# Kernel optimization log

Hardware: AMD Instinct MI355X
Metric: run time of the kernel (lower is better)

The kernel has to match this reference:

```python
import jax, jax.numpy as jnp
import numpy as np

M, K = 16384, 1024
E, N = 8, 5632  # N = 2 * intermediate (gate+up packed); intermediate = 2816
TOPK = 2


def setup_inputs() -> dict:
    key = jax.random.key(0)
    ks = jax.random.split(key, 5)
    return {
        "hidden_states": jax.random.normal(ks[0], (M, K), jnp.float32) * 0.05,
        "w1": jax.random.normal(ks[1], (E, N, K), jnp.float32) * 0.02,
        "w2": jax.random.normal(ks[2], (E, K, N // 2), jnp.float32) * 0.02,
        "topk_weights": jax.random.uniform(ks[3], (M, TOPK), jnp.float32),
        "topk_ids": jax.random.randint(ks[4], (M, TOPK), 0, E, jnp.int32),
    }


def reference(hidden_states, w1, w2, topk_weights, topk_ids):
    # hidden_states: [M, K]; w1: [E, N, K]; w2: [E, K, N//2]
    # topk_weights / topk_ids: [M, TOPK]
    m, k = hidden_states.shape
    e_num, n, _ = w1.shape
    topk = topk_ids.shape[1]
    half = n // 2
    out = jnp.zeros((m, topk, k), dtype=hidden_states.dtype)
    # Loop over the small fixed set of experts; each iteration is a dense GEMM
    # masked by the routing assignment (faithful to the grouped-GEMM math).
    for e in range(e_num):
        h1 = jnp.einsum('mk,nk->mn', hidden_states, w1[e])          # [M, N]
        gate, up = h1[:, :half], h1[:, half:]
        h2 = jax.nn.silu(gate) * up                                  # silu_and_mul
        o = jnp.einsum('mh,kh->mk', h2, w2[e])                       # [M, K]
        mask = (topk_ids == e).astype(o.dtype)                       # [M, TOPK]
        out = out + mask[:, :, None] * o[:, None, :]
    # multiply routed weights and sum over top-k slots
    return jnp.einsum('mtk,mt->mk', out, topk_weights)
```

## Files before the change

### kernel.cpp

```cpp
#include <hip/hip_runtime.h>
#include <hip/hip_bf16.h>

#define M_TOK 16384
#define K_DIM 1024
#define E_NUM 8
#define N_DIM 5632
#define HALF_N 2816
#define TOPK 2
#define NPAIR (M_TOK * TOPK)
#define BM 128
#define BK 64
#define BH1 128
#define BN 128
#define NDESC (NPAIR / BM + E_NUM)
#define NHB1 (HALF_N / BH1)
#define NNB2 (K_DIM / BN)

typedef short s16x4 __attribute__((ext_vector_type(4)));
typedef short s16x8 __attribute__((ext_vector_type(8)));
typedef float f32x4 __attribute__((ext_vector_type(4)));

__device__ __forceinline__ short f2bf(float f) {
  union { __hip_bfloat16 h; short s; } c;
  c.h = __float2bfloat16(f);
  return c.s;
}

__device__ __forceinline__ float bf2f(unsigned short s) {
  union { float f; unsigned u; } c;
  c.u = ((unsigned)s) << 16;
  return c.f;
}

__device__ __forceinline__ void gload_lds16(const void* g, void* l) {
  __builtin_amdgcn_global_load_lds(
      (const __attribute__((address_space(1))) unsigned int*)g,
      (__attribute__((address_space(3))) unsigned int*)l, 16, 0, 0);
}

__device__ __forceinline__ int xcd_work(int bid, int nwg) {
  const int xcd = bid & 7, loc = bid >> 3;
  const int q = nwg >> 3, r = nwg & 7;
  return (xcd < r ? xcd * (q + 1) : r * (q + 1) + (xcd - r) * q) + loc;
}

__global__ void cvt_f32_bf16_k(const float4* __restrict__ src,
                               s16x4* __restrict__ dst, int n4) {
  int i = blockIdx.x * blockDim.x + threadIdx.x;
  int stride = gridDim.x * blockDim.x;
  for (; i < n4; i += stride) {
    float4 f = src[i];
    s16x4 o = { f2bf(f.x), f2bf(f.y), f2bf(f.z), f2bf(f.w) };
    dst[i] = o;
  }
}

__global__ void moe_count(const int* __restrict__ ids, int* __restrict__ cnt) {
  const int p = blockIdx.x * 256 + threadIdx.x;
  const int e = ids[p];
  const int lane = threadIdx.x & 63;
  __shared__ int h[E_NUM];
  if (threadIdx.x < E_NUM) h[threadIdx.x] = 0;
  __syncthreads();
#pragma unroll
  for (int ex = 0; ex < E_NUM; ++ex) {
    unsigned long long m = __ballot(e == ex);
    if (lane == 0 && m) atomicAdd(&h[ex], __popcll(m));
  }
  __syncthreads();
  if (threadIdx.x < E_NUM) atomicAdd(&cnt[threadIdx.x], h[threadIdx.x]);
}

__global__ void moe_build(const int* __restrict__ cnt, int* __restrict__ offs,
                          int4* __restrict__ desc) {
  if (blockIdx.x == 0 && threadIdx.x == 0) {
    int o = 0, d = 0;
    for (int e = 0; e < E_NUM; ++e) {
      offs[e] = o;
      int end = o + cnt[e];
      for (int s = o; s < end; s += BM) desc[d++] = make_int4(e, s, end, 0);
      o = end;
    }
    offs[E_NUM] = o;
    while (d < NDESC) desc[d++] = make_int4(-1, 0, 0, 0);
  }
}

__global__ void moe_scatter(const int* __restrict__ ids, const float* __restrict__ tw,
                            const int* __restrict__ offs, int* __restrict__ fill,
                            int* __restrict__ tok, float* __restrict__ wgt,
                            int* __restrict__ inv) {
  const int p = blockIdx.x * 256 + threadIdx.x;
  const int e = ids[p];
  const int lane = threadIdx.x & 63;
  const int w = threadIdx.x >> 6;
  __shared__ int wcnt[4][E_NUM];
  __shared__ int wpre[4][E_NUM];
  __shared__ int base[E_NUM];
  const unsigned long long lt = (1ull << lane) - 1ull;
  int myrank = 0;
#pragma unroll
  for (int ex = 0; ex < E_NUM; ++ex) {
    unsigned long long m = __ballot(e == ex);
    if (e == ex) myrank = (int)__popcll(m & lt);
    if (lane == 0) wcnt[w][ex] = (int)__popcll(m);
  }
  __syncthreads();
  if (threadIdx.x < E_NUM) {
    const int ex = threadIdx.x;
    int s = 0;
#pragma unroll
    for (int ww = 0; ww < 4; ++ww) { wpre[ww][ex] = s; s += wcnt[ww][ex]; }
    base[ex] = atomicAdd(&fill[ex], s);
  }
  __syncthreads();
  const int pos = offs[e] + base[e] + wpre[w][e] + myrank;
  tok[pos] = p >> 1;
  wgt[pos] = tw[p];
  inv[p] = pos;
}

__global__ void moe_gather(const float* __restrict__ hs, const int* __restrict__ tok,
                           unsigned short* __restrict__ hsb) {
  const int pos = blockIdx.x;
  const int m = tok[pos];
  const int t = threadIdx.x;
  const float4* s = (const float4*)(hs + (size_t)m * K_DIM) + t * 2;
  const float4 a = s[0], b = s[1];
  s16x8 o = { f2bf(a.x), f2bf(a.y), f2bf(a.z), f2bf(a.w),
              f2bf(b.x), f2bf(b.y), f2bf(b.z), f2bf(b.w) };
  *(s16x8*)(hsb + (size_t)pos * K_DIM + t * 8) = o;
}

__launch_bounds__(512)
__global__ void moe_gemm1(const unsigned short* __restrict__ hsb,
                          const unsigned short* __restrict__ w1b,
                          const int4* __restrict__ desc,
                          unsigned short* __restrict__ h2) {
  const int work = xcd_work(blockIdx.x, NHB1 * NDESC);
  const int di = work / NHB1;
  const int hb = work - di * NHB1;
  const int4 d = desc[di];
  const int e = d.x;
  if (e < 0) return;
  const int pos0 = d.y, eend = d.z;
  const int h0 = hb * BH1;

  __shared__ __align__(16) unsigned short As[BM * BK];
  __shared__ __align__(16) unsigned short Gs[BH1 * BK];
  __shared__ __align__(16) unsigned short Us[BH1 * BK];

  const int tid = threadIdx.x;
  const int lane = tid & 63;
  const int wid = tid >> 6;
  const int wr = wid >> 2;
  const int wc = wid & 3;

  const unsigned short* Ab = hsb + (size_t)pos0 * K_DIM;
  const unsigned short* Gb = w1b + ((size_t)e * N_DIM + h0) * K_DIM;
  const unsigned short* Ub = Gb + (size_t)HALF_N * K_DIM;

  f32x4 accg[4][2], accu[4][2];
  const f32x4 z = {0.f, 0.f, 0.f, 0.f};
#pragma unroll
  for (int i = 0; i < 4; ++i)
#pragma unroll
    for (int j = 0; j < 2; ++j) { accg[i][j] = z; accu[i][j] = z; }

  const int lrow = lane >> 3;
  const int scol = ((lane & 7) ^ lrow) << 3;
  const int fr = lane & 15;
  const int fq = lane >> 4;
  const int sw = fr & 7;

  for (int kt = 0; kt < K_DIM / BK; ++kt) {
    const int k0 = kt * BK;
#pragma unroll
    for (int c = 0; c < 2; ++c) {
      const int seg = c * 8 + wid;
      const int row = seg * 8 + lrow;
      gload_lds16(Ab + (size_t)row * K_DIM + k0 + scol, &As[seg * 512]);
      gload_lds16(Gb + (size_t)row * K_DIM + k0 + scol, &Gs[seg * 512]);
      gload_lds16(Ub + (size_t)row * K_DIM + k0 + scol, &Us[seg * 512]);
    }
    __syncthreads();
#pragma unroll
    for (int s = 0; s < 2; ++s) {
      const int coff = (((s * 4 + fq) ^ sw) << 3);
      s16x8 af[4];
#pragma unroll
      for (int i = 0; i < 4; ++i)
        af[i] = *(const s16x8*)&As[(64 * wr + 16 * i + fr) * BK + coff];
      s16x8 gf[2], uf[2];
#pragma unroll
      for (int j = 0; j < 2; ++j) {
        const int hr = (32 * wc + 16 * j + fr) * BK + coff;
        gf[j] = *(const s16x8*)&Gs[hr];
        uf[j] = *(const s16x8*)&Us[hr];
      }
#pragma unroll
      for (int i = 0; i < 4; ++i)
#pragma unroll
        for (int j = 0; j < 2; ++j) {
          accg[i][j] = __builtin_amdgcn_mfma_f32_16x16x32_bf16(af[i], gf[j], accg[i][j], 0, 0, 0);
          accu[i][j] = __builtin_amdgcn_mfma_f32_16x16x32_bf16(af[i], uf[j], accu[i][j], 0, 0, 0);
        }
    }
    __syncthreads();
  }

  const int vlim = eend - pos0;
#pragma unroll
  for (int i = 0; i < 4; ++i) {
#pragma unroll
    for (int rr = 0; rr < 4; ++rr) {
      const int row = 64 * wr + 16 * i + fq * 4 + rr;
      if (row < vlim) {
        unsigned short* dst = h2 + (size_t)(pos0 + row) * HALF_N + h0 + 32 * wc;
#pragma unroll
        for (int j = 0; j < 2; ++j) {
          const float g = accg[i][j][rr];
          const float u = accu[i][j][rr];
          const float sg = g / (1.0f + __expf(-g));
          dst[16 * j + fr] = (unsigned short)f2bf(sg * u);
        }
      }
    }
  }
}

__launch_bounds__(256)
__global__ void moe_gemm2(const unsigned short* __restrict__ h2,
                          const unsigned short* __restrict__ w2b,
                          const int4* __restrict__ desc,
                          const float* __restrict__ wgt,
                          unsigned short* __restrict__ opair) {
  const int work = xcd_work(blockIdx.x, NNB2 * NDESC);
  const int di = work >> 3;
  const int nb = work & 7;
  const int4 d = desc[di];
  const int e = d.x;
  if (e < 0) return;
  const int pos0 = d.y, eend = d.z;
  const int n0 = nb * BN;

  __shared__ __align__(16) unsigned short As[BM * BK];
  __shared__ __align__(16) unsigned short Bs[BN * BK];

  const int tid = threadIdx.x;
  const int lane = tid & 63;
  const int wid = tid >> 6;
  const int wr = wid >> 1, wc = wid & 1;

  const unsigned short* Ab = h2 + (size_t)pos0 * HALF_N;
  const unsigned short* Bb = w2b + ((size_t)e * K_DIM + n0) * HALF_N;

  f32x4 acc[4][4];
  const f32x4 z = {0.f, 0.f, 0.f, 0.f};
#pragma unroll
  for (int i = 0; i < 4; ++i)
#pragma unroll
    for (int j = 0; j < 4; ++j) acc[i][j] = z;

  const int lrow = lane >> 3;
  const int scol = ((lane & 7) ^ lrow) << 3;
  const int fr = lane & 15;
  const int fq = lane >> 4;
  const int sw = fr & 7;

  for (int ht = 0; ht < HALF_N / BK; ++ht) {
    const int k0 = ht * BK;
#pragma unroll
    for (int c = 0; c < 4; ++c) {
      const int seg = c * 4 + wid;
      const int row = seg * 8 + lrow;
      gload_lds16(Ab + (size_t)row * HALF_N + k0 + scol, &As[seg * 512]);
      gload_lds16(Bb + (size_t)row * HALF_N + k0 + scol, &Bs[seg * 512]);
    }
    __syncthreads();
#pragma unroll
    for (int s = 0; s < 2; ++s) {
      const int coff = (((s * 4 + fq) ^ sw) << 3);
      s16x8 af[4], bf[4];
#pragma unroll
      for (int i = 0; i < 4; ++i)
        af[i] = *(const s16x8*)&As[(64 * wr + 16 * i + fr) * BK + coff];
#pragma unroll
      for (int j = 0; j < 4; ++j)
        bf[j] = *(const s16x8*)&Bs[(64 * wc + 16 * j + fr) * BK + coff];
#pragma unroll
      for (int i = 0; i < 4; ++i)
#pragma unroll
        for (int j = 0; j < 4; ++j)
          acc[i][j] = __builtin_amdgcn_mfma_f32_16x16x32_bf16(af[i], bf[j], acc[i][j], 0, 0, 0);
    }
    __syncthreads();
  }

  const int vlim = eend - pos0;
#pragma unroll
  for (int i = 0; i < 4; ++i) {
#pragma unroll
    for (int rr = 0; rr < 4; ++rr) {
      const int row = 64 * wr + 16 * i + fq * 4 + rr;
      if (row < vlim) {
        const int pos = pos0 + row;
        const float wt = wgt[pos];
        unsigned short* dst = opair + (size_t)pos * K_DIM + n0 + 64 * wc;
#pragma unroll
        for (int j = 0; j < 4; ++j)
          dst[16 * j + fr] = (unsigned short)f2bf(wt * acc[i][j][rr]);
      }
    }
  }
}

__global__ void moe_combine(const unsigned short* __restrict__ opair,
                            const int* __restrict__ inv,
                            float* __restrict__ out) {
  const int m = blockIdx.x;
  const int t = threadIdx.x;
  const int p0 = inv[2 * m], p1 = inv[2 * m + 1];
  const s16x8 a = *(const s16x8*)&opair[(size_t)p0 * K_DIM + t * 8];
  const s16x8 b = *(const s16x8*)&opair[(size_t)p1 * K_DIM + t * 8];
  float4 o0, o1;
  o0.x = bf2f((unsigned short)a[0]) + bf2f((unsigned short)b[0]);
  o0.y = bf2f((unsigned short)a[1]) + bf2f((unsigned short)b[1]);
  o0.z = bf2f((unsigned short)a[2]) + bf2f((unsigned short)b[2]);
  o0.w = bf2f((unsigned short)a[3]) + bf2f((unsigned short)b[3]);
  o1.x = bf2f((unsigned short)a[4]) + bf2f((unsigned short)b[4]);
  o1.y = bf2f((unsigned short)a[5]) + bf2f((unsigned short)b[5]);
  o1.z = bf2f((unsigned short)a[6]) + bf2f((unsigned short)b[6]);
  o1.w = bf2f((unsigned short)a[7]) + bf2f((unsigned short)b[7]);
  float4* dst = (float4*)(out + (size_t)m * K_DIM + t * 8);
  dst[0] = o0;
  dst[1] = o1;
}

__global__ void sentinel_k(float* o) { o[0] = 1.0e9f; }

extern "C" void kernel_launch(void* const* d_in, const int* in_sizes, int n_in,
                              void* d_out, int out_size, void* d_ws, size_t ws_size,
                              hipStream_t stream) {
  const float* hs = (const float*)d_in[0];
  const float* w1 = (const float*)d_in[1];
  const float* w2 = (const float*)d_in[2];
  const float* tw = (const float*)d_in[3];
  const int* ids = (const int*)d_in[4];
  float* out = (float*)d_out;

  char* p = (char*)d_ws;
  auto carve = [&](size_t bytes) {
    char* r = p;
    p += (bytes + 255) & ~(size_t)255;
    return r;
  };
  unsigned short* w1b = (unsigned short*)carve((size_t)E_NUM * N_DIM * K_DIM * 2);
  unsigned short* w2b = (unsigned short*)carve((size_t)E_NUM * K_DIM * HALF_N * 2);
  unsigned short* hsb = (unsigned short*)carve((size_t)(NPAIR + BM) * K_DIM * 2);
  unsigned short* h2  = (unsigned short*)carve((size_t)(NPAIR + BM) * HALF_N * 2);
  int*   tok  = (int*)carve(NPAIR * 4);
  float* wgt  = (float*)carve(NPAIR * 4);
  int*   inv  = (int*)carve(NPAIR * 4);
  int*   meta = (int*)carve(1024);
  int4*  desc = (int4*)carve(NDESC * sizeof(int4));
  size_t need = (size_t)(p - (char*)d_ws);

  unsigned short* opair = hsb;

  if (need > ws_size) {
    hipMemsetAsync(d_out, 0, (size_t)out_size * sizeof(float), stream);
    sentinel_k<<<1, 1, 0, stream>>>(out);
    return;
  }

  int* cnt  = meta;
  int* fill = meta + 64;
  int* offs = meta + 128;

  hipMemsetAsync(meta, 0, 1024, stream);

  cvt_f32_bf16_k<<<2048, 256, 0, stream>>>(
      (const float4*)w1, (s16x4*)w1b, (int)((size_t)E_NUM * N_DIM * K_DIM / 4));
  cvt_f32_bf16_k<<<2048, 256, 0, stream>>>(
      (const float4*)w2, (s16x4*)w2b, (int)((size_t)E_NUM * K_DIM * HALF_N / 4));
  moe_count<<<NPAIR / 256, 256, 0, stream>>>(ids, cnt);
  moe_build<<<1, 64, 0, stream>>>(cnt, offs, desc);
  moe_scatter<<<NPAIR / 256, 256, 0, stream>>>(ids, tw, offs, fill, tok, wgt, inv);
  moe_gather<<<NPAIR, 128, 0, stream>>>(hs, tok, hsb);
  moe_gemm1<<<NHB1 * NDESC, 512, 0, stream>>>(hsb, w1b, desc, h2);
  moe_gemm2<<<NNB2 * NDESC, 256, 0, stream>>>(h2, w2b, desc, wgt, opair);
  moe_combine<<<M_TOK, 128, 0, stream>>>(opair, inv, out);
}
```

Before: 907.4 us.

## Restructure gemm1 with 256-row tiles and a 4-buffer software-pipelined K loop

The first grouped GEMM now uses 256-token tiles with its own descriptor list, and gate and up rows are interleaved into a single B tile. The K loop is 32 wide and runs over a 4-stage LDS ring, prefetching two steps ahead with explicit vmcnt waits, barriers and s_setprio around the MFMA bursts. The aim is to overlap global-to-LDS loads with matrix work and to double A/B reuse per block, cutting weight reloads. The costs are more padding waste on expert tails, a larger accumulator footprint of 128 floats per lane, and hand-tuned sync that may be fragile.

```diff
diff --git a/kernel.cpp b/kernel.cpp
--- a/kernel.cpp
+++ b/kernel.cpp
@@ -8,12 +8,14 @@
 #define HALF_N 2816
 #define TOPK 2
 #define NPAIR (M_TOK * TOPK)
+#define BM1 256
+#define BH1 128
+#define NHB1 (HALF_N / BH1)
+#define NDESC1 (NPAIR / BM1 + E_NUM)
 #define BM 128
 #define BK 64
-#define BH1 128
 #define BN 128
-#define NDESC (NPAIR / BM + E_NUM)
-#define NHB1 (HALF_N / BH1)
+#define NDESC2 (NPAIR / BM + E_NUM)
 #define NNB2 (K_DIM / BN)
 
 typedef short s16x4 __attribute__((ext_vector_type(4)));
@@ -72,17 +74,19 @@
 }
 
 __global__ void moe_build(const int* __restrict__ cnt, int* __restrict__ offs,
-                          int4* __restrict__ desc) {
+                          int4* __restrict__ desc1, int4* __restrict__ desc2) {
   if (blockIdx.x == 0 && threadIdx.x == 0) {
-    int o = 0, d = 0;
+    int o = 0, d1 = 0, d2 = 0;
     for (int e = 0; e < E_NUM; ++e) {
       offs[e] = o;
       int end = o + cnt[e];
-      for (int s = o; s < end; s += BM) desc[d++] = make_int4(e, s, end, 0);
+      for (int s = o; s < end; s += BM1) desc1[d1++] = make_int4(e, s, end, 0);
+      for (int s = o; s < end; s += BM)  desc2[d2++] = make_int4(e, s, end, 0);
       o = end;
     }
     offs[E_NUM] = o;
-    while (d < NDESC) desc[d++] = make_int4(-1, 0, 0, 0);
+    while (d1 < NDESC1) desc1[d1++] = make_int4(-1, 0, 0, 0);
+    while (d2 < NDESC2) desc2[d2++] = make_int4(-1, 0, 0, 0);
   }
 }
 
@@ -135,94 +139,113 @@
 __launch_bounds__(512)
 __global__ void moe_gemm1(const unsigned short* __restrict__ hsb,
                           const unsigned short* __restrict__ w1b,
-                          const int4* __restrict__ desc,
+                          const int4* __restrict__ desc1,
                           unsigned short* __restrict__ h2) {
-  const int work = xcd_work(blockIdx.x, NHB1 * NDESC);
+  const int work = xcd_work(blockIdx.x, NHB1 * NDESC1);
   const int di = work / NHB1;
   const int hb = work - di * NHB1;
-  const int4 d = desc[di];
+  const int4 d = desc1[di];
   const int e = d.x;
   if (e < 0) return;
   const int pos0 = d.y, eend = d.z;
   const int h0 = hb * BH1;
 
-  __shared__ __align__(16) unsigned short As[BM * BK];
-  __shared__ __align__(16) unsigned short Gs[BH1 * BK];
-  __shared__ __align__(16) unsigned short Us[BH1 * BK];
+  __shared__ __align__(16) unsigned short As[4][BM1 * 32];
+  __shared__ __align__(16) unsigned short Bs[4][BM1 * 32];
 
   const int tid = threadIdx.x;
   const int lane = tid & 63;
   const int wid = tid >> 6;
   const int wr = wid >> 2;
   const int wc = wid & 3;
-
-  const unsigned short* Ab = hsb + (size_t)pos0 * K_DIM;
-  const unsigned short* Gb = w1b + ((size_t)e * N_DIM + h0) * K_DIM;
-  const unsigned short* Ub = Gb + (size_t)HALF_N * K_DIM;
-
-  f32x4 accg[4][2], accu[4][2];
-  const f32x4 z = {0.f, 0.f, 0.f, 0.f};
-#pragma unroll
-  for (int i = 0; i < 4; ++i)
-#pragma unroll
-    for (int j = 0; j < 2; ++j) { accg[i][j] = z; accu[i][j] = z; }
-
-  const int lrow = lane >> 3;
-  const int scol = ((lane & 7) ^ lrow) << 3;
   const int fr = lane & 15;
   const int fq = lane >> 4;
-  const int sw = fr & 7;
-
-  for (int kt = 0; kt < K_DIM / BK; ++kt) {
-    const int k0 = kt * BK;
-#pragma unroll
-    for (int c = 0; c < 2; ++c) {
-      const int seg = c * 8 + wid;
-      const int row = seg * 8 + lrow;
-      gload_lds16(Ab + (size_t)row * K_DIM + k0 + scol, &As[seg * 512]);
-      gload_lds16(Gb + (size_t)row * K_DIM + k0 + scol, &Gs[seg * 512]);
-      gload_lds16(Ub + (size_t)row * K_DIM + k0 + scol, &Us[seg * 512]);
-    }
-    __syncthreads();
-#pragma unroll
-    for (int s = 0; s < 2; ++s) {
-      const int coff = (((s * 4 + fq) ^ sw) << 3);
-      s16x8 af[4];
-#pragma unroll
-      for (int i = 0; i < 4; ++i)
-        af[i] = *(const s16x8*)&As[(64 * wr + 16 * i + fr) * BK + coff];
-      s16x8 gf[2], uf[2];
-#pragma unroll
-      for (int j = 0; j < 2; ++j) {
-        const int hr = (32 * wc + 16 * j + fr) * BK + coff;
-        gf[j] = *(const s16x8*)&Gs[hr];
-        uf[j] = *(const s16x8*)&Us[hr];
-      }
-#pragma unroll
-      for (int i = 0; i < 4; ++i)
-#pragma unroll
-        for (int j = 0; j < 2; ++j) {
-          accg[i][j] = __builtin_amdgcn_mfma_f32_16x16x32_bf16(af[i], gf[j], accg[i][j], 0, 0, 0);
-          accu[i][j] = __builtin_amdgcn_mfma_f32_16x16x32_bf16(af[i], uf[j], accu[i][j], 0, 0, 0);
-        }
-    }
-    __syncthreads();
+
+  const int srow = tid >> 2;
+  const int schunk = (tid & 3) ^ ((tid >> 3) & 3);
+  const unsigned short* AgA = hsb + (size_t)(pos0 + srow) * K_DIM + schunk * 8;
+  const unsigned short* AgB = hsb + (size_t)(pos0 + 128 + srow) * K_DIM + schunk * 8;
+  const int br0 = srow, br1 = 128 + srow;
+  const int grow0 = h0 + ((br0 >> 5) << 4) + (br0 & 15) + (((br0 >> 4) & 1) ? HALF_N : 0);
+  const int grow1 = h0 + ((br1 >> 5) << 4) + (br1 & 15) + (((br1 >> 4) & 1) ? HALF_N : 0);
+  const unsigned short* BgA = w1b + ((size_t)e * N_DIM + grow0) * K_DIM + schunk * 8;
+  const unsigned short* BgB = w1b + ((size_t)e * N_DIM + grow1) * K_DIM + schunk * 8;
+
+  auto STAGE_A = [&](int b, int kt) {
+    const int k0 = kt * 32;
+    gload_lds16(AgA + k0, &As[b][tid * 8]);
+    gload_lds16(AgB + k0, &As[b][4096 + tid * 8]);
+  };
+  auto STAGE_B = [&](int b, int kt) {
+    const int k0 = kt * 32;
+    gload_lds16(BgA + k0, &Bs[b][tid * 8]);
+    gload_lds16(BgB + k0, &Bs[b][4096 + tid * 8]);
+  };
+
+  f32x4 acc[8][4];
+  const f32x4 z = {0.f, 0.f, 0.f, 0.f};
+#pragma unroll
+  for (int i = 0; i < 8; ++i)
+#pragma unroll
+    for (int j = 0; j < 4; ++j) acc[i][j] = z;
+
+  const int coff = ((fq ^ ((fr >> 1) & 3)) << 3);
+  const int abase = (wr * 128 + fr) * 32 + coff;
+  const int bbase = (wc * 64 + fr) * 32 + coff;
+
+  const int NT = K_DIM / 32;
+  STAGE_A(0, 0); STAGE_B(0, 0);
+  STAGE_A(1, 1); STAGE_B(1, 1);
+  asm volatile("s_waitcnt vmcnt(4)\n\ts_barrier" ::: "memory");
+
+  for (int t = 0; t < NT; ++t) {
+    const int b = t & 3;
+    const int nb = (t + 2) & 3;
+    const bool pf = (t + 2) < NT;
+    s16x8 afv[4], bfv[4];
+#pragma unroll
+    for (int i = 0; i < 4; ++i) afv[i] = *(const s16x8*)&As[b][abase + i * 512];
+#pragma unroll
+    for (int j = 0; j < 4; ++j) bfv[j] = *(const s16x8*)&Bs[b][bbase + j * 512];
+    if (pf) STAGE_A(nb, t + 2);
+    asm volatile("s_barrier" ::: "memory");
+    __builtin_amdgcn_s_setprio(1);
+#pragma unroll
+    for (int i = 0; i < 4; ++i)
+#pragma unroll
+      for (int j = 0; j < 4; ++j)
+        acc[i][j] = __builtin_amdgcn_mfma_f32_16x16x32_bf16(afv[i], bfv[j], acc[i][j], 0, 0, 0);
+    __builtin_amdgcn_s_setprio(0);
+    asm volatile("s_barrier" ::: "memory");
+#pragma unroll
+    for (int i = 0; i < 4; ++i) afv[i] = *(const s16x8*)&As[b][abase + (4 + i) * 512];
+    if (pf) STAGE_B(nb, t + 2);
+    asm volatile("s_barrier" ::: "memory");
+    __builtin_amdgcn_s_setprio(1);
+#pragma unroll
+    for (int i = 0; i < 4; ++i)
+#pragma unroll
+      for (int j = 0; j < 4; ++j)
+        acc[4 + i][j] = __builtin_amdgcn_mfma_f32_16x16x32_bf16(afv[i], bfv[j], acc[4 + i][j], 0, 0, 0);
+    __builtin_amdgcn_s_setprio(0);
+    if (pf) asm volatile("s_waitcnt vmcnt(4)\n\ts_barrier" ::: "memory");
+    else    asm volatile("s_waitcnt vmcnt(0)\n\ts_barrier" ::: "memory");
   }
 
   const int vlim = eend - pos0;
 #pragma unroll
-  for (int i = 0; i < 4; ++i) {
+  for (int i = 0; i < 8; ++i) {
 #pragma unroll
     for (int rr = 0; rr < 4; ++rr) {
-      const int row = 64 * wr + 16 * i + fq * 4 + rr;
+      const int row = wr * 128 + i * 16 + fq * 4 + rr;
       if (row < vlim) {
         unsigned short* dst = h2 + (size_t)(pos0 + row) * HALF_N + h0 + 32 * wc;
 #pragma unroll
-        for (int j = 0; j < 2; ++j) {
-          const float g = accg[i][j][rr];
-          const float u = accu[i][j][rr];
+        for (int jp = 0; jp < 2; ++jp) {
+          const float g = acc[i][2 * jp][rr];
+          const float u = acc[i][2 * jp + 1][rr];
           const float sg = g / (1.0f + __expf(-g));
-          dst[16 * j + fr] = (unsigned short)f2bf(sg * u);
+          dst[jp * 16 + fr] = (unsigned short)f2bf(sg * u);
         }
       }
     }
@@ -232,13 +255,13 @@
 __launch_bounds__(256)
 __global__ void moe_gemm2(const unsigned short* __restrict__ h2,
                           const unsigned short* __restrict__ w2b,
-                          const int4* __restrict__ desc,
+                          const int4* __restrict__ desc2,
                           const float* __restrict__ wgt,
                           unsigned short* __restrict__ opair) {
-  const int work = xcd_work(blockIdx.x, NNB2 * NDESC);
+  const int work = xcd_work(blockIdx.x, NNB2 * NDESC2);
   const int di = work >> 3;
   const int nb = work & 7;
-  const int4 d = desc[di];
+  const int4 d = desc2[di];
   const int e = d.x;
   if (e < 0) return;
   const int pos0 = d.y, eend = d.z;
@@ -309,7 +332,7 @@
         unsigned short* dst = opair + (size_t)pos * K_DIM + n0 + 64 * wc;
 #pragma unroll
         for (int j = 0; j < 4; ++j)
-          dst[16 * j + fr] = (unsigned short)f2bf(wt * acc[i][j][rr]);
+          dst[16 * j + fr] = (unsigned short)f2bf(wt * acc[i][rr == rr ? j : j][rr]);
       }
     }
   }
@@ -357,13 +380,14 @@
   };
   unsigned short* w1b = (unsigned short*)carve((size_t)E_NUM * N_DIM * K_DIM * 2);
   unsigned short* w2b = (unsigned short*)carve((size_t)E_NUM * K_DIM * HALF_N * 2);
-  unsigned short* hsb = (unsigned short*)carve((size_t)(NPAIR + BM) * K_DIM * 2);
-  unsigned short* h2  = (unsigned short*)carve((size_t)(NPAIR + BM) * HALF_N * 2);
+  unsigned short* hsb = (unsigned short*)carve((size_t)(NPAIR + BM1) * K_DIM * 2);
+  unsigned short* h2  = (unsigned short*)carve((size_t)(NPAIR + BM1) * HALF_N * 2);
   int*   tok  = (int*)carve(NPAIR * 4);
   float* wgt  = (float*)carve(NPAIR * 4);
   int*   inv  = (int*)carve(NPAIR * 4);
   int*   meta = (int*)carve(1024);
-  int4*  desc = (int4*)carve(NDESC * sizeof(int4));
+  int4*  desc1 = (int4*)carve(NDESC1 * sizeof(int4));
+  int4*  desc2 = (int4*)carve(NDESC2 * sizeof(int4));
   size_t need = (size_t)(p - (char*)d_ws);
 
   unsigned short* opair = hsb;
@@ -385,10 +409,10 @@
   cvt_f32_bf16_k<<<2048, 256, 0, stream>>>(
       (const float4*)w2, (s16x4*)w2b, (int)((size_t)E_NUM * K_DIM * HALF_N / 4));
   moe_count<<<NPAIR / 256, 256, 0, stream>>>(ids, cnt);
-  moe_build<<<1, 64, 0, stream>>>(cnt, offs, desc);
+  moe_build<<<1, 64, 0, stream>>>(cnt, offs, desc1, desc2);
   moe_scatter<<<NPAIR / 256, 256, 0, stream>>>(ids, tw, offs, fill, tok, wgt, inv);
   moe_gather<<<NPAIR, 128, 0, stream>>>(hs, tok, hsb);
-  moe_gemm1<<<NHB1 * NDESC, 512, 0, stream>>>(hsb, w1b, desc, h2);
-  moe_gemm2<<<NNB2 * NDESC, 256, 0, stream>>>(h2, w2b, desc, wgt, opair);
+  moe_gemm1<<<NHB1 * NDESC1, 512, 0, stream>>>(hsb, w1b, desc1, h2);
+  moe_gemm2<<<NNB2 * NDESC2, 256, 0, stream>>>(h2, w2b, desc2, wgt, opair);
   moe_combine<<<M_TOK, 128, 0, stream>>>(opair, inv, out);
 }
```

After: 948.3 us. 4.5% more time.
